# Optimization experiments

Hardware: AMD Instinct MI355X
Metric: run time of the kernel (lower is better)

Reference implementation:

```python
import jax, jax.numpy as jnp
import numpy as np

B, A, L, D, H = 8, 16, 80, 128, 6  # scenes, agents/scene, lanes/scene, feat dim, heads
LN_EPS = 1e-5


def _build_edges():
    hi_l, wi_l = [], []
    n_agt = B * A
    for b in range(B):
        ids = np.concatenate([np.arange(b * A, (b + 1) * A),
                              n_agt + np.arange(b * L, (b + 1) * L)])
        n = len(ids)
        hi_l.append(np.repeat(ids, n))  # 'd -> (d n)'
        wi_l.append(np.tile(ids, n))    # 'd -> (n d)'
    return (jnp.asarray(np.concatenate(hi_l), dtype=jnp.int32),
            jnp.asarray(np.concatenate(wi_l), dtype=jnp.int32))


def setup_inputs() -> dict:
    key = jax.random.key(0)
    ks = jax.random.split(key, 10)
    w = 0.05  # small init so exp(att) is well-behaved
    hi, wi = _build_edges()
    return {
        "agents": jax.random.normal(ks[0], (B * A, D), jnp.float32),
        "lanes": jax.random.normal(ks[1], (B * L, D), jnp.float32),
        "Wq": w * jax.random.normal(ks[2], (D, H * D), jnp.float32),
        "Wk": w * jax.random.normal(ks[3], (D, H * D), jnp.float32),
        "Wv": w * jax.random.normal(ks[4], (D, H * D), jnp.float32),
        "Wout1": w * jax.random.normal(ks[5], (H * D, D), jnp.float32),
        "Wout2": w * jax.random.normal(ks[6], (D, D), jnp.float32),
        "W1": w * jax.random.normal(ks[7], (D, D), jnp.float32),
        "ln_g": jnp.ones((D,), jnp.float32),
        "ln_b": jnp.zeros((D,), jnp.float32),
        "W2": w * jax.random.normal(ks[8], (D, D), jnp.float32),
        "hi": hi,
        "wi": wi,
    }


def _layernorm(x, g, b):
    mu = x.mean(-1, keepdims=True)
    var = ((x - mu) ** 2).mean(-1, keepdims=True)
    return (x - mu) * jax.lax.rsqrt(var + LN_EPS) * g + b


def reference(agents, lanes, Wq, Wk, Wv, Wout1, Wout2, W1, ln_g, ln_b, W2, hi, wi):
    nodes = jnp.concatenate([agents, lanes], axis=0)  # [N, D]
    N = nodes.shape[0]
    n_agt = agents.shape[0]
    scale = D ** -0.5

    src = nodes[hi]  # [E, D] (query side)
    dst = nodes[wi]  # [E, D] (key/value side)
    q = (src @ Wq).reshape(-1, H, D)
    k = (dst @ Wk).reshape(-1, H, D)
    v = jax.nn.relu(dst @ Wv).reshape(-1, H, D)

    att = jnp.einsum('ehd,ehd->eh', q, k) * scale          # [E, H]
    att = jnp.exp(att - att.max())                          # global-max-shifted exp (as in source)
    denom = jax.ops.segment_sum(att, hi, num_segments=N)    # [N, H]
    att = att / denom[hi]
    out = jax.ops.segment_sum(att[..., None] * v, hi, num_segments=N)  # [N, H, D]
    out = out.reshape(N, H * D)

    out = jax.nn.relu(out @ Wout1) @ Wout2                  # to_out
    h = _layernorm(nodes @ W1 + out, ln_g, ln_b)
    h = jax.nn.relu(h)
    h = h @ W2
    h = jax.nn.relu(h + nodes)                              # residual to pre-attention nodes
    return h[:n_agt]
```

## Files before the change

kernel.cpp:

```cpp
#include <hip/hip_runtime.h>
#include <math.h>

#define LN_EPS 1e-5f


__global__ __launch_bounds__(256) void k_qv(
    const float* __restrict__ agents, const float* __restrict__ lanes,
    const float* __restrict__ Wv, const float* __restrict__ Wq,
    const float* __restrict__ W1, float* __restrict__ V,
    float* __restrict__ Qb, float* __restrict__ base)
{
    __shared__ float As[128][68];
    __shared__ float Bs[128][68];

    const int tid = threadIdx.x;
    const int bid = blockIdx.x;

    const float* W;
    float* Out;
    int r0, wc0, wstride, dstride;
    bool dorelu = false;
    if (bid < 144) {
        const int br = bid % 12, bc = bid / 12;
        r0 = br * 64; W = Wv; wc0 = bc * 64; wstride = 768;
        Out = V; dstride = 768; dorelu = true;
    } else if (bid < 168) {
        const int idx = bid - 144;
        r0 = (idx & 1) * 64; W = Wq; wc0 = (idx >> 1) * 64; wstride = 768;
        Out = Qb; dstride = 768;
    } else {
        const int idx = bid - 168;
        r0 = (idx & 1) * 64; W = W1; wc0 = (idx >> 1) * 64; wstride = 128;
        Out = base; dstride = 128;
    }

    {
        const int row = tid >> 2, kv = tid & 3;
        const int gr = r0 + row;
        const float* src = (gr < 128) ? (agents + (size_t)gr * 128)
                                      : (lanes + (size_t)(gr - 128) * 128);
        #pragma unroll
        for (int j = 0; j < 8; ++j) {
            const int k0 = kv * 4 + j * 16;
            const float4 a = *(const float4*)(src + k0);
            As[k0 + 0][row] = a.x; As[k0 + 1][row] = a.y;
            As[k0 + 2][row] = a.z; As[k0 + 3][row] = a.w;
        }
    }
    {
        const int kr = tid >> 4, c4 = tid & 15;
        #pragma unroll
        for (int i = 0; i < 8; ++i) {
            const int k = kr + 16 * i;
            *(float4*)&Bs[k][c4 * 4] =
                *(const float4*)(W + (size_t)k * wstride + wc0 + c4 * 4);
        }
    }
    __syncthreads();

    const int tx = tid & 15, ty = tid >> 4;
    float acc[4][4] = {};
    #pragma unroll 8
    for (int k = 0; k < 128; ++k) {
        const float4 a = *(const float4*)&As[k][ty * 4];
        const float4 b = *(const float4*)&Bs[k][tx * 4];
        const float av[4] = {a.x, a.y, a.z, a.w};
        #pragma unroll
        for (int i = 0; i < 4; ++i) {
            acc[i][0] += av[i] * b.x; acc[i][1] += av[i] * b.y;
            acc[i][2] += av[i] * b.z; acc[i][3] += av[i] * b.w;
        }
    }
    #pragma unroll
    for (int i = 0; i < 4; ++i) {
        float4 v = make_float4(acc[i][0], acc[i][1], acc[i][2], acc[i][3]);
        if (dorelu) {
            v.x = fmaxf(v.x, 0.f); v.y = fmaxf(v.y, 0.f);
            v.z = fmaxf(v.z, 0.f); v.w = fmaxf(v.w, 0.f);
        }
        *(float4*)(Out + (size_t)(r0 + ty * 4 + i) * dstride + wc0 + tx * 4) = v;
    }
}

__global__ __launch_bounds__(512) void k_attn2(
    const float* __restrict__ agents, const float* __restrict__ lanes,
    const float* __restrict__ Wk, const float* __restrict__ V,
    const float* __restrict__ Qb, float* __restrict__ AO)
{
    __shared__ float Ns[96][132];
    __shared__ float Vh[96][68];
    __shared__ float Qs[16][132];
    __shared__ float Tt[16][132];
    __shared__ float Sm[16][100];
    __shared__ float Wc[32][132];

    const int tid = threadIdx.x;
    const int b = blockIdx.x;
    const int s = b / 12, r12 = b % 12;
    const int h = r12 >> 1, half = r12 & 1;

    #pragma unroll
    for (int ii = 0; ii < 6; ++ii) {
        const int idx = tid + ii * 512;
        const int n = idx >> 5, c4 = idx & 31;
        const float* src = (n < 16) ? (agents + (size_t)(s * 16 + n) * 128)
                                    : (lanes + (size_t)(s * 80 + n - 16) * 128);
        *(float4*)&Ns[n][c4 * 4] = *(const float4*)(src + c4 * 4);
    }
    #pragma unroll
    for (int ii = 0; ii < 3; ++ii) {
        const int idx = tid + ii * 512;
        const int n = idx >> 4, c4 = idx & 15;
        const int g = (n < 16) ? (s * 16 + n) : (128 + s * 80 + (n - 16));
        *(float4*)&Vh[n][c4 * 4] =
            *(const float4*)(V + (size_t)g * 768 + h * 128 + half * 64 + c4 * 4);
    }
    {
        const int r = tid >> 5, c4 = tid & 31;
        *(float4*)&Qs[r][c4 * 4] =
            *(const float4*)(Qb + (size_t)(s * 16 + r) * 768 + h * 128 + c4 * 4);
    }
    __syncthreads();

    const int r = tid >> 5, kc = tid & 31;
    for (int ck = 0; ck < 4; ++ck) {
        {
            const int i0 = tid * 2;
            #pragma unroll
            for (int ii = 0; ii < 2; ++ii) {
                const int idx = i0 + ii;
                const int row = idx >> 5, c4 = idx & 31;
                *(float4*)&Wc[row][c4 * 4] =
                    *(const float4*)(Wk + (size_t)(ck * 32 + row) * 768 +
                                     h * 128 + c4 * 4);
            }
        }
        __syncthreads();
        {
            float acc = 0.f;
            #pragma unroll 8
            for (int c4 = 0; c4 < 32; ++c4) {
                const float4 q = *(const float4*)&Qs[r][c4 * 4];
                const float4 w = *(const float4*)&Wc[kc][c4 * 4];
                acc += q.x * w.x + q.y * w.y + q.z * w.z + q.w * w.w;
            }
            Tt[r][ck * 32 + kc] = acc;
        }
        __syncthreads();
    }

    {
        const int i = r, jc = kc;
        float s0 = 0, s1 = 0, s2 = 0;
        #pragma unroll 4
        for (int kk = 0; kk < 32; ++kk) {
            const float4 t4 = *(const float4*)&Tt[i][kk * 4];
            const float4 a  = *(const float4*)&Ns[jc][kk * 4];
            const float4 bb = *(const float4*)&Ns[jc + 32][kk * 4];
            const float4 c  = *(const float4*)&Ns[jc + 64][kk * 4];
            s0 += t4.x*a.x  + t4.y*a.y  + t4.z*a.z  + t4.w*a.w;
            s1 += t4.x*bb.x + t4.y*bb.y + t4.z*bb.z + t4.w*bb.w;
            s2 += t4.x*c.x  + t4.y*c.y  + t4.z*c.z  + t4.w*c.w;
        }
        const float scale = 0.088388347648318447f;
        s0 *= scale; s1 *= scale; s2 *= scale;
        float m = fmaxf(fmaxf(s0, s1), s2);
        #pragma unroll
        for (int o = 16; o >= 1; o >>= 1) m = fmaxf(m, __shfl_xor(m, o, 32));
        const float e0 = __expf(s0 - m), e1 = __expf(s1 - m), e2 = __expf(s2 - m);
        float sum = e0 + e1 + e2;
        #pragma unroll
        for (int o = 16; o >= 1; o >>= 1) sum += __shfl_xor(sum, o, 32);
        const float inv = 1.0f / sum;
        Sm[i][jc]      = e0 * inv;
        Sm[i][jc + 32] = e1 * inv;
        Sm[i][jc + 64] = e2 * inv;
    }

    {
        const int i = r, d = kc;
        float o0 = 0, o1 = 0;
        #pragma unroll 4
        for (int j = 0; j < 96; ++j) {
            const float p = Sm[i][j];
            const float2 v = *(const float2*)&Vh[j][2 * d];
            o0 += p * v.x; o1 += p * v.y;
        }
        float* dst = AO + (size_t)(s * 16 + i) * 768 + h * 128 + half * 64 + 2 * d;
        *(float2*)dst = make_float2(o0, o1);
    }
}

__global__ __launch_bounds__(256) void k_f1w(
    const float* __restrict__ AO, const float* __restrict__ Wout1,
    float* __restrict__ y1p)
{
    __shared__ float As[64][68];
    __shared__ float Bs[64][68];

    const int tid = threadIdx.x;
    const int b = blockIdx.x;
    const int ks = b >> 2, quad = b & 3;
    const int m0 = (quad >> 1) * 64, n0 = (quad & 1) * 64;

    {
        const int row = tid >> 2, kq = tid & 3;
        #pragma unroll
        for (int j = 0; j < 4; ++j) {
            const int k0 = kq * 4 + j * 16;
            const float4 a =
                *(const float4*)(AO + (size_t)(m0 + row) * 768 + ks * 64 + k0);
            As[k0 + 0][row] = a.x; As[k0 + 1][row] = a.y;
            As[k0 + 2][row] = a.z; As[k0 + 3][row] = a.w;
        }
    }
    {
        const int kr = tid >> 4, c4 = tid & 15;
        #pragma unroll
        for (int i = 0; i < 4; ++i) {
            const int k = kr + 16 * i;
            *(float4*)&Bs[k][c4 * 4] =
                *(const float4*)(Wout1 + (size_t)(ks * 64 + k) * 128 + n0 + c4 * 4);
        }
    }
    __syncthreads();

    const int tx = tid & 15, ty = tid >> 4;
    float acc[4][4] = {};
    #pragma unroll 8
    for (int k = 0; k < 64; ++k) {
        const float4 a = *(const float4*)&As[k][ty * 4];
        const float4 bv = *(const float4*)&Bs[k][tx * 4];
        const float av[4] = {a.x, a.y, a.z, a.w};
        #pragma unroll
        for (int i = 0; i < 4; ++i) {
            acc[i][0] += av[i] * bv.x; acc[i][1] += av[i] * bv.y;
            acc[i][2] += av[i] * bv.z; acc[i][3] += av[i] * bv.w;
        }
    }
    float* dst = y1p + (size_t)ks * 16384 + (size_t)m0 * 128 + n0;
    #pragma unroll
    for (int i = 0; i < 4; ++i)
        *(float4*)(dst + (size_t)(ty * 4 + i) * 128 + tx * 4) =
            make_float4(acc[i][0], acc[i][1], acc[i][2], acc[i][3]);
}

__global__ __launch_bounds__(512) void k_f2(
    const float* __restrict__ y1p, const float* __restrict__ base,
    const float* __restrict__ agents, const float* __restrict__ Wout2,
    const float* __restrict__ ln_g, const float* __restrict__ ln_b,
    const float* __restrict__ W2, float* __restrict__ out)
{
    const int a = blockIdx.x;
    const int tid = threadIdx.x;
    __shared__ float y1s[128];
    __shared__ float nr[128];
    __shared__ float br[128];
    __shared__ float hb[128];
    __shared__ float ps[512];
    __shared__ float red[4];

    if (tid < 32) {
        float4 acc = make_float4(0,0,0,0);
        #pragma unroll
        for (int ks = 0; ks < 12; ++ks) {
            const float4 v =
                *(const float4*)(y1p + (size_t)ks * 16384 + (size_t)a * 128 + tid * 4);
            acc.x += v.x; acc.y += v.y; acc.z += v.z; acc.w += v.w;
        }
        y1s[tid * 4 + 0] = fmaxf(acc.x, 0.f); y1s[tid * 4 + 1] = fmaxf(acc.y, 0.f);
        y1s[tid * 4 + 2] = fmaxf(acc.z, 0.f); y1s[tid * 4 + 3] = fmaxf(acc.w, 0.f);
    } else if (tid < 64) {
        const int t = tid - 32;
        *(float4*)&nr[t * 4] = *(const float4*)(agents + (size_t)a * 128 + t * 4);
    } else if (tid < 96) {
        const int t = tid - 64;
        *(float4*)&br[t * 4] = *(const float4*)(base + (size_t)a * 128 + t * 4);
    }
    __syncthreads();

    const int d = tid & 127, g = tid >> 7;
    {
        const int k0 = g * 32;
        float p = 0.f;
        #pragma unroll 8
        for (int k = 0; k < 32; ++k)
            p += y1s[k0 + k] * Wout2[(size_t)(k0 + k) * 128 + d];
        ps[tid] = p;
    }
    __syncthreads();

    float tval = 0.f;
    if (tid < 128) tval = ps[d] + ps[128 + d] + ps[256 + d] + ps[384 + d] + br[d];
    float s1 = tval, s2 = tval * tval;
    #pragma unroll
    for (int o = 32; o >= 1; o >>= 1) { s1 += __shfl_xor(s1, o); s2 += __shfl_xor(s2, o); }
    if (tid < 128 && (tid & 63) == 0) {
        red[(tid >> 6) * 2] = s1; red[(tid >> 6) * 2 + 1] = s2;
    }
    __syncthreads();
    if (tid < 128) {
        const float S1 = red[0] + red[2], S2 = red[1] + red[3];
        const float mu  = S1 * (1.0f / 128.0f);
        const float var = S2 * (1.0f / 128.0f) - mu * mu;
        const float rin = rsqrtf(var + LN_EPS);
        hb[tid] = fmaxf((tval - mu) * rin * ln_g[tid] + ln_b[tid], 0.0f);
    }
    __syncthreads();

    {
        const int k0 = g * 32;
        float p = 0.f;
        #pragma unroll 8
        for (int k = 0; k < 32; ++k)
            p += hb[k0 + k] * W2[(size_t)(k0 + k) * 128 + d];
        ps[tid] = p;
    }
    __syncthreads();
    if (tid < 128)
        out[(size_t)a * 128 + d] =
            fmaxf(ps[d] + ps[128 + d] + ps[256 + d] + ps[384 + d] + nr[d], 0.0f);
}

extern "C" void kernel_launch(void* const* d_in, const int* in_sizes, int n_in,
                              void* d_out, int out_size, void* d_ws, size_t ws_size,
                              hipStream_t stream)
{
    const float* agents = (const float*)d_in[0];
    const float* lanes  = (const float*)d_in[1];
    const float* Wq     = (const float*)d_in[2];
    const float* Wk     = (const float*)d_in[3];
    const float* Wv     = (const float*)d_in[4];
    const float* Wout1  = (const float*)d_in[5];
    const float* Wout2  = (const float*)d_in[6];
    const float* W1     = (const float*)d_in[7];
    const float* ln_g   = (const float*)d_in[8];
    const float* ln_b   = (const float*)d_in[9];
    const float* W2     = (const float*)d_in[10];

    float* ws = (float*)d_ws;
    float* V    = ws;
    float* Qb   = V + 768 * 768;
    float* base = Qb + 128 * 768;
    float* AO   = base + 16384;
    float* y1p  = AO + 128 * 768;
    float* outp = (float*)d_out;

    k_qv   <<<172, 256, 0, stream>>>(agents, lanes, Wv, Wq, W1, V, Qb, base);
    k_attn2<<<96, 512, 0, stream>>>(agents, lanes, Wk, V, Qb, AO);
    k_f1w  <<<48, 256, 0, stream>>>(AO, Wout1, y1p);
    k_f2   <<<128, 512, 0, stream>>>(y1p, base, agents, Wout2, ln_g, ln_b, W2, outp);
}
```

Before: 108.6 us.

## Fuse all stages into one cooperative kernel with grid sync

Replaces the four launches with a single cooperative kernel. Each attention block now computes its own V and Q projections in shared memory instead of reading them from precomputed global buffers. A grid-wide sync follows, after which 64 blocks each run the Wout1/Wout2/W1/LayerNorm/W2 tail for two agents. This removes three launch boundaries and the V/Qb/base/y1p workspace traffic. In exchange, V is recomputed per head-half tile, the Wout1 GEMM runs on fewer blocks with uncoalesced-per-thread weight reads, and the grid sync adds cost.

```diff
diff --git a/kernel.cpp b/kernel.cpp
--- a/kernel.cpp
+++ b/kernel.cpp
@@ -1,325 +1,287 @@
 #include <hip/hip_runtime.h>
+#include <hip/hip_cooperative_groups.h>
 #include <math.h>
 
 #define LN_EPS 1e-5f
 
-
-__global__ __launch_bounds__(256) void k_qv(
+namespace cg = cooperative_groups;
+
+
+#define RELU4(v) do { (v).x=fmaxf((v).x,0.f); (v).y=fmaxf((v).y,0.f); \
+                      (v).z=fmaxf((v).z,0.f); (v).w=fmaxf((v).w,0.f); } while(0)
+
+__global__ __launch_bounds__(512) void k_fused(
     const float* __restrict__ agents, const float* __restrict__ lanes,
-    const float* __restrict__ Wv, const float* __restrict__ Wq,
-    const float* __restrict__ W1, float* __restrict__ V,
-    float* __restrict__ Qb, float* __restrict__ base)
+    const float* __restrict__ Wq, const float* __restrict__ Wk,
+    const float* __restrict__ Wv, const float* __restrict__ Wout1,
+    const float* __restrict__ Wout2, const float* __restrict__ W1,
+    const float* __restrict__ ln_g, const float* __restrict__ ln_b,
+    const float* __restrict__ W2, float* __restrict__ AO,
+    float* __restrict__ out)
 {
-    __shared__ float As[128][68];
-    __shared__ float Bs[128][68];
-
-    const int tid = threadIdx.x;
-    const int bid = blockIdx.x;
-
-    const float* W;
-    float* Out;
-    int r0, wc0, wstride, dstride;
-    bool dorelu = false;
-    if (bid < 144) {
-        const int br = bid % 12, bc = bid / 12;
-        r0 = br * 64; W = Wv; wc0 = bc * 64; wstride = 768;
-        Out = V; dstride = 768; dorelu = true;
-    } else if (bid < 168) {
-        const int idx = bid - 144;
-        r0 = (idx & 1) * 64; W = Wq; wc0 = (idx >> 1) * 64; wstride = 768;
-        Out = Qb; dstride = 768;
-    } else {
-        const int idx = bid - 168;
-        r0 = (idx & 1) * 64; W = W1; wc0 = (idx >> 1) * 64; wstride = 128;
-        Out = base; dstride = 128;
-    }
-
-    {
-        const int row = tid >> 2, kv = tid & 3;
-        const int gr = r0 + row;
-        const float* src = (gr < 128) ? (agents + (size_t)gr * 128)
-                                      : (lanes + (size_t)(gr - 128) * 128);
-        #pragma unroll
-        for (int j = 0; j < 8; ++j) {
-            const int k0 = kv * 4 + j * 16;
-            const float4 a = *(const float4*)(src + k0);
-            As[k0 + 0][row] = a.x; As[k0 + 1][row] = a.y;
-            As[k0 + 2][row] = a.z; As[k0 + 3][row] = a.w;
-        }
-    }
-    {
-        const int kr = tid >> 4, c4 = tid & 15;
-        #pragma unroll
-        for (int i = 0; i < 8; ++i) {
-            const int k = kr + 16 * i;
-            *(float4*)&Bs[k][c4 * 4] =
-                *(const float4*)(W + (size_t)k * wstride + wc0 + c4 * 4);
-        }
-    }
-    __syncthreads();
-
-    const int tx = tid & 15, ty = tid >> 4;
-    float acc[4][4] = {};
-    #pragma unroll 8
-    for (int k = 0; k < 128; ++k) {
-        const float4 a = *(const float4*)&As[k][ty * 4];
-        const float4 b = *(const float4*)&Bs[k][tx * 4];
-        const float av[4] = {a.x, a.y, a.z, a.w};
-        #pragma unroll
-        for (int i = 0; i < 4; ++i) {
-            acc[i][0] += av[i] * b.x; acc[i][1] += av[i] * b.y;
-            acc[i][2] += av[i] * b.z; acc[i][3] += av[i] * b.w;
-        }
-    }
-    #pragma unroll
-    for (int i = 0; i < 4; ++i) {
-        float4 v = make_float4(acc[i][0], acc[i][1], acc[i][2], acc[i][3]);
-        if (dorelu) {
-            v.x = fmaxf(v.x, 0.f); v.y = fmaxf(v.y, 0.f);
-            v.z = fmaxf(v.z, 0.f); v.w = fmaxf(v.w, 0.f);
-        }
-        *(float4*)(Out + (size_t)(r0 + ty * 4 + i) * dstride + wc0 + tx * 4) = v;
-    }
-}
-
-__global__ __launch_bounds__(512) void k_attn2(
-    const float* __restrict__ agents, const float* __restrict__ lanes,
-    const float* __restrict__ Wk, const float* __restrict__ V,
-    const float* __restrict__ Qb, float* __restrict__ AO)
-{
-    __shared__ float Ns[96][132];
-    __shared__ float Vh[96][68];
-    __shared__ float Qs[16][132];
-    __shared__ float Tt[16][132];
-    __shared__ float Sm[16][100];
-    __shared__ float Wc[32][132];
+    __shared__ float smem[29248];
 
     const int tid = threadIdx.x;
     const int b = blockIdx.x;
-    const int s = b / 12, r12 = b % 12;
-    const int h = r12 >> 1, half = r12 & 1;
-
-    #pragma unroll
-    for (int ii = 0; ii < 6; ++ii) {
-        const int idx = tid + ii * 512;
-        const int n = idx >> 5, c4 = idx & 31;
-        const float* src = (n < 16) ? (agents + (size_t)(s * 16 + n) * 128)
-                                    : (lanes + (size_t)(s * 80 + n - 16) * 128);
-        *(float4*)&Ns[n][c4 * 4] = *(const float4*)(src + c4 * 4);
-    }
-    #pragma unroll
-    for (int ii = 0; ii < 3; ++ii) {
-        const int idx = tid + ii * 512;
-        const int n = idx >> 4, c4 = idx & 15;
-        const int g = (n < 16) ? (s * 16 + n) : (128 + s * 80 + (n - 16));
-        *(float4*)&Vh[n][c4 * 4] =
-            *(const float4*)(V + (size_t)g * 768 + h * 128 + half * 64 + c4 * 4);
-    }
+
     {
-        const int r = tid >> 5, c4 = tid & 31;
-        *(float4*)&Qs[r][c4 * 4] =
-            *(const float4*)(Qb + (size_t)(s * 16 + r) * 768 + h * 128 + c4 * 4);
-    }
-    __syncthreads();
-
-    const int r = tid >> 5, kc = tid & 31;
-    for (int ck = 0; ck < 4; ++ck) {
-        {
-            const int i0 = tid * 2;
+        float (*Ns)[132] = (float (*)[132])(smem);
+        float (*Vh)[68]  = (float (*)[68]) (smem + 12672);
+        float (*Qs)[132] = (float (*)[132])(smem + 19200);
+        float (*Tt)[132] = (float (*)[132])(smem + 21312);
+        float (*Sm)[100] = (float (*)[100])(smem + 23424);
+        float (*Wc)[132] = (float (*)[132])(smem + 25024);
+
+        const int sc = b / 12, r12 = b % 12;
+        const int h = r12 >> 1, half = r12 & 1;
+
+        #pragma unroll
+        for (int ii = 0; ii < 6; ++ii) {
+            const int idx = tid + ii * 512;
+            const int n = idx >> 5, c4 = idx & 31;
+            const float* src = (n < 16) ? (agents + (size_t)(sc * 16 + n) * 128)
+                                        : (lanes + (size_t)(sc * 80 + n - 16) * 128);
+            *(float4*)&Ns[n][c4 * 4] = *(const float4*)(src + c4 * 4);
+        }
+
+        {
+            const int r = tid >> 4, c4 = tid & 15;
+            float4 acc0 = make_float4(0, 0, 0, 0);
+            float4 acc1 = make_float4(0, 0, 0, 0);
+            float4 acc2 = make_float4(0, 0, 0, 0);
+            for (int ck = 0; ck < 4; ++ck) {
+                *(float4*)&Wc[r][c4 * 4] = *(const float4*)(
+                    Wv + (size_t)(ck * 32 + r) * 768 + h * 128 + half * 64 + c4 * 4);
+                __syncthreads();
+                #pragma unroll
+                for (int kk = 0; kk < 8; ++kk) {
+                    const int k0 = ck * 32 + kk * 4;
+                    const float4 n0 = *(const float4*)&Ns[r     ][k0];
+                    const float4 n1 = *(const float4*)&Ns[r + 32][k0];
+                    const float4 n2 = *(const float4*)&Ns[r + 64][k0];
+                    const float a0[4] = {n0.x, n0.y, n0.z, n0.w};
+                    const float a1[4] = {n1.x, n1.y, n1.z, n1.w};
+                    const float a2[4] = {n2.x, n2.y, n2.z, n2.w};
+                    #pragma unroll
+                    for (int j = 0; j < 4; ++j) {
+                        const float4 w = *(const float4*)&Wc[kk * 4 + j][c4 * 4];
+                        acc0.x += a0[j]*w.x; acc0.y += a0[j]*w.y;
+                        acc0.z += a0[j]*w.z; acc0.w += a0[j]*w.w;
+                        acc1.x += a1[j]*w.x; acc1.y += a1[j]*w.y;
+                        acc1.z += a1[j]*w.z; acc1.w += a1[j]*w.w;
+                        acc2.x += a2[j]*w.x; acc2.y += a2[j]*w.y;
+                        acc2.z += a2[j]*w.z; acc2.w += a2[j]*w.w;
+                    }
+                }
+                __syncthreads();
+            }
+            RELU4(acc0); RELU4(acc1); RELU4(acc2);
+            *(float4*)&Vh[r     ][c4 * 4] = acc0;
+            *(float4*)&Vh[r + 32][c4 * 4] = acc1;
+            *(float4*)&Vh[r + 64][c4 * 4] = acc2;
+        }
+
+        {
+            const int r = tid >> 5, kc = tid & 31;
+            float4 acc = make_float4(0, 0, 0, 0);
+            for (int ck = 0; ck < 4; ++ck) {
+                #pragma unroll
+                for (int ii = 0; ii < 2; ++ii) {
+                    const int idx = tid * 2 + ii;
+                    const int row = idx >> 5, cc = idx & 31;
+                    *(float4*)&Wc[row][cc * 4] = *(const float4*)(
+                        Wq + (size_t)(ck * 32 + row) * 768 + h * 128 + cc * 4);
+                }
+                __syncthreads();
+                #pragma unroll
+                for (int kk = 0; kk < 8; ++kk) {
+                    const float4 qa = *(const float4*)&Ns[r][ck * 32 + kk * 4];
+                    const float av[4] = {qa.x, qa.y, qa.z, qa.w};
+                    #pragma unroll
+                    for (int j = 0; j < 4; ++j) {
+                        const float4 w = *(const float4*)&Wc[kk * 4 + j][kc * 4];
+                        acc.x += av[j]*w.x; acc.y += av[j]*w.y;
+                        acc.z += av[j]*w.z; acc.w += av[j]*w.w;
+                    }
+                }
+                __syncthreads();
+            }
+            *(float4*)&Qs[r][kc * 4] = acc;
+        }
+
+        const int r = tid >> 5, kc = tid & 31;
+        for (int ck = 0; ck < 4; ++ck) {
             #pragma unroll
             for (int ii = 0; ii < 2; ++ii) {
-                const int idx = i0 + ii;
-                const int row = idx >> 5, c4 = idx & 31;
-                *(float4*)&Wc[row][c4 * 4] =
-                    *(const float4*)(Wk + (size_t)(ck * 32 + row) * 768 +
-                                     h * 128 + c4 * 4);
-            }
-        }
-        __syncthreads();
-        {
-            float acc = 0.f;
+                const int idx = tid * 2 + ii;
+                const int row = idx >> 5, cc = idx & 31;
+                *(float4*)&Wc[row][cc * 4] = *(const float4*)(
+                    Wk + (size_t)(ck * 32 + row) * 768 + h * 128 + cc * 4);
+            }
+            __syncthreads();
+            {
+                float acc = 0.f;
+                #pragma unroll 8
+                for (int c4 = 0; c4 < 32; ++c4) {
+                    const float4 q = *(const float4*)&Qs[r][c4 * 4];
+                    const float4 w = *(const float4*)&Wc[kc][c4 * 4];
+                    acc += q.x*w.x + q.y*w.y + q.z*w.z + q.w*w.w;
+                }
+                Tt[r][ck * 32 + kc] = acc;
+            }
+            __syncthreads();
+        }
+
+        {
+            const int i = r, jc = kc;
+            float s0 = 0, s1 = 0, s2 = 0;
+            #pragma unroll 4
+            for (int kk = 0; kk < 32; ++kk) {
+                const float4 t4 = *(const float4*)&Tt[i][kk * 4];
+                const float4 a  = *(const float4*)&Ns[jc][kk * 4];
+                const float4 bb = *(const float4*)&Ns[jc + 32][kk * 4];
+                const float4 c  = *(const float4*)&Ns[jc + 64][kk * 4];
+                s0 += t4.x*a.x  + t4.y*a.y  + t4.z*a.z  + t4.w*a.w;
+                s1 += t4.x*bb.x + t4.y*bb.y + t4.z*bb.z + t4.w*bb.w;
+                s2 += t4.x*c.x  + t4.y*c.y  + t4.z*c.z  + t4.w*c.w;
+            }
+            const float scale = 0.088388347648318447f;
+            s0 *= scale; s1 *= scale; s2 *= scale;
+            float m = fmaxf(fmaxf(s0, s1), s2);
+            #pragma unroll
+            for (int o = 16; o >= 1; o >>= 1) m = fmaxf(m, __shfl_xor(m, o, 32));
+            const float e0 = __expf(s0 - m), e1 = __expf(s1 - m), e2 = __expf(s2 - m);
+            float sum = e0 + e1 + e2;
+            #pragma unroll
+            for (int o = 16; o >= 1; o >>= 1) sum += __shfl_xor(sum, o, 32);
+            const float inv = 1.0f / sum;
+            Sm[i][jc]      = e0 * inv;
+            Sm[i][jc + 32] = e1 * inv;
+            Sm[i][jc + 64] = e2 * inv;
+        }
+
+        {
+            const int i = r, dd = kc;
+            float o0 = 0, o1 = 0;
+            #pragma unroll 4
+            for (int j = 0; j < 96; ++j) {
+                const float p = Sm[i][j];
+                const float2 v = *(const float2*)&Vh[j][2 * dd];
+                o0 += p * v.x; o1 += p * v.y;
+            }
+            float* dst = AO + (size_t)(sc * 16 + i) * 768 + h * 128 + half * 64 + 2 * dd;
+            *(float2*)dst = make_float2(o0, o1);
+        }
+    }
+
+    __threadfence();
+    cg::this_grid().sync();
+
+    if (b < 64) {
+        float* ao0 = smem;
+        float* ao1 = smem + 768;
+        float* ps0 = smem + 1536;
+        float* ps1 = smem + 2048;
+        float* y10 = smem + 2560;
+        float* y11 = smem + 2688;
+        float* nr0 = smem + 2816;
+        float* nr1 = smem + 2944;
+        float* hb0 = smem + 3072;
+        float* hb1 = smem + 3200;
+        float* red = smem + 3328;
+
+        const int a0 = b * 2, a1 = b * 2 + 1;
+        if (tid < 192) {
+            *(float4*)&ao0[tid * 4] = *(const float4*)(AO + (size_t)a0 * 768 + tid * 4);
+        } else if (tid < 384) {
+            const int t = tid - 192;
+            *(float4*)&ao1[t * 4] = *(const float4*)(AO + (size_t)a1 * 768 + t * 4);
+        } else if (tid < 416) {
+            const int t = tid - 384;
+            *(float4*)&nr0[t * 4] = *(const float4*)(agents + (size_t)a0 * 128 + t * 4);
+        } else if (tid < 448) {
+            const int t = tid - 416;
+            *(float4*)&nr1[t * 4] = *(const float4*)(agents + (size_t)a1 * 128 + t * 4);
+        }
+        __syncthreads();
+
+        const int d = tid & 127, g = tid >> 7;
+        {
+            float p0 = 0.f, p1 = 0.f;
+            const int k0 = g * 192;
             #pragma unroll 8
-            for (int c4 = 0; c4 < 32; ++c4) {
-                const float4 q = *(const float4*)&Qs[r][c4 * 4];
-                const float4 w = *(const float4*)&Wc[kc][c4 * 4];
-                acc += q.x * w.x + q.y * w.y + q.z * w.z + q.w * w.w;
-            }
-            Tt[r][ck * 32 + kc] = acc;
-        }
-        __syncthreads();
+            for (int k = 0; k < 192; ++k) {
+                const float w = Wout1[(size_t)(k0 + k) * 128 + d];
+                p0 += ao0[k0 + k] * w; p1 += ao1[k0 + k] * w;
+            }
+            ps0[tid] = p0; ps1[tid] = p1;
+        }
+        __syncthreads();
+        if (tid < 128) {
+            y10[tid] = fmaxf(ps0[tid] + ps0[128 + tid] + ps0[256 + tid] + ps0[384 + tid], 0.f);
+            y11[tid] = fmaxf(ps1[tid] + ps1[128 + tid] + ps1[256 + tid] + ps1[384 + tid], 0.f);
+        }
+        __syncthreads();
+        {
+            float p0 = 0.f, p1 = 0.f;
+            const int k0 = g * 32;
+            #pragma unroll 8
+            for (int k = 0; k < 32; ++k) {
+                const float w2v = Wout2[(size_t)(k0 + k) * 128 + d];
+                const float w1v = W1[(size_t)(k0 + k) * 128 + d];
+                p0 += y10[k0 + k] * w2v + nr0[k0 + k] * w1v;
+                p1 += y11[k0 + k] * w2v + nr1[k0 + k] * w1v;
+            }
+            ps0[tid] = p0; ps1[tid] = p1;
+        }
+        __syncthreads();
+        float t0 = 0.f, t1 = 0.f;
+        if (tid < 128) {
+            t0 = ps0[d] + ps0[128 + d] + ps0[256 + d] + ps0[384 + d];
+            t1 = ps1[d] + ps1[128 + d] + ps1[256 + d] + ps1[384 + d];
+        }
+        float s10 = t0, s20 = t0 * t0, s11 = t1, s21 = t1 * t1;
+        #pragma unroll
+        for (int o = 32; o >= 1; o >>= 1) {
+            s10 += __shfl_xor(s10, o); s20 += __shfl_xor(s20, o);
+            s11 += __shfl_xor(s11, o); s21 += __shfl_xor(s21, o);
+        }
+        if (tid < 128 && (tid & 63) == 0) {
+            const int wid = tid >> 6;
+            red[wid * 4 + 0] = s10; red[wid * 4 + 1] = s20;
+            red[wid * 4 + 2] = s11; red[wid * 4 + 3] = s21;
+        }
+        __syncthreads();
+        if (tid < 128) {
+            const float S10 = red[0] + red[4], S20 = red[1] + red[5];
+            const float S11 = red[2] + red[6], S21 = red[3] + red[7];
+            const float mu0 = S10 * (1.0f / 128.0f);
+            const float var0 = S20 * (1.0f / 128.0f) - mu0 * mu0;
+            const float mu1 = S11 * (1.0f / 128.0f);
+            const float var1 = S21 * (1.0f / 128.0f) - mu1 * mu1;
+            const float g_ = ln_g[tid], b_ = ln_b[tid];
+            hb0[tid] = fmaxf((t0 - mu0) * rsqrtf(var0 + LN_EPS) * g_ + b_, 0.0f);
+            hb1[tid] = fmaxf((t1 - mu1) * rsqrtf(var1 + LN_EPS) * g_ + b_, 0.0f);
+        }
+        __syncthreads();
+        {
+            float p0 = 0.f, p1 = 0.f;
+            const int k0 = g * 32;
+            #pragma unroll 8
+            for (int k = 0; k < 32; ++k) {
+                const float w = W2[(size_t)(k0 + k) * 128 + d];
+                p0 += hb0[k0 + k] * w; p1 += hb1[k0 + k] * w;
+            }
+            ps0[tid] = p0; ps1[tid] = p1;
+        }
+        __syncthreads();
+        if (tid < 128) {
+            out[(size_t)a0 * 128 + d] =
+                fmaxf(ps0[d] + ps0[128 + d] + ps0[256 + d] + ps0[384 + d] + nr0[d], 0.0f);
+            out[(size_t)a1 * 128 + d] =
+                fmaxf(ps1[d] + ps1[128 + d] + ps1[256 + d] + ps1[384 + d] + nr1[d], 0.0f);
+        }
     }
-
-    {
-        const int i = r, jc = kc;
-        float s0 = 0, s1 = 0, s2 = 0;
-        #pragma unroll 4
-        for (int kk = 0; kk < 32; ++kk) {
-            const float4 t4 = *(const float4*)&Tt[i][kk * 4];
-            const float4 a  = *(const float4*)&Ns[jc][kk * 4];
-            const float4 bb = *(const float4*)&Ns[jc + 32][kk * 4];
-            const float4 c  = *(const float4*)&Ns[jc + 64][kk * 4];
-            s0 += t4.x*a.x  + t4.y*a.y  + t4.z*a.z  + t4.w*a.w;
-            s1 += t4.x*bb.x + t4.y*bb.y + t4.z*bb.z + t4.w*bb.w;
-            s2 += t4.x*c.x  + t4.y*c.y  + t4.z*c.z  + t4.w*c.w;
-        }
-        const float scale = 0.088388347648318447f;
-        s0 *= scale; s1 *= scale; s2 *= scale;
-        float m = fmaxf(fmaxf(s0, s1), s2);
-        #pragma unroll
-        for (int o = 16; o >= 1; o >>= 1) m = fmaxf(m, __shfl_xor(m, o, 32));
-        const float e0 = __expf(s0 - m), e1 = __expf(s1 - m), e2 = __expf(s2 - m);
-        float sum = e0 + e1 + e2;
-        #pragma unroll
-        for (int o = 16; o >= 1; o >>= 1) sum += __shfl_xor(sum, o, 32);
-        const float inv = 1.0f / sum;
-        Sm[i][jc]      = e0 * inv;
-        Sm[i][jc + 32] = e1 * inv;
-        Sm[i][jc + 64] = e2 * inv;
-    }
-
-    {
-        const int i = r, d = kc;
-        float o0 = 0, o1 = 0;
-        #pragma unroll 4
-        for (int j = 0; j < 96; ++j) {
-            const float p = Sm[i][j];
-            const float2 v = *(const float2*)&Vh[j][2 * d];
-            o0 += p * v.x; o1 += p * v.y;
-        }
-        float* dst = AO + (size_t)(s * 16 + i) * 768 + h * 128 + half * 64 + 2 * d;
-        *(float2*)dst = make_float2(o0, o1);
-    }
-}
-
-__global__ __launch_bounds__(256) void k_f1w(
-    const float* __restrict__ AO, const float* __restrict__ Wout1,
-    float* __restrict__ y1p)
-{
-    __shared__ float As[64][68];
-    __shared__ float Bs[64][68];
-
-    const int tid = threadIdx.x;
-    const int b = blockIdx.x;
-    const int ks = b >> 2, quad = b & 3;
-    const int m0 = (quad >> 1) * 64, n0 = (quad & 1) * 64;
-
-    {
-        const int row = tid >> 2, kq = tid & 3;
-        #pragma unroll
-        for (int j = 0; j < 4; ++j) {
-            const int k0 = kq * 4 + j * 16;
-            const float4 a =
-                *(const float4*)(AO + (size_t)(m0 + row) * 768 + ks * 64 + k0);
-            As[k0 + 0][row] = a.x; As[k0 + 1][row] = a.y;
-            As[k0 + 2][row] = a.z; As[k0 + 3][row] = a.w;
-        }
-    }
-    {
-        const int kr = tid >> 4, c4 = tid & 15;
-        #pragma unroll
-        for (int i = 0; i < 4; ++i) {
-            const int k = kr + 16 * i;
-            *(float4*)&Bs[k][c4 * 4] =
-                *(const float4*)(Wout1 + (size_t)(ks * 64 + k) * 128 + n0 + c4 * 4);
-        }
-    }
-    __syncthreads();
-
-    const int tx = tid & 15, ty = tid >> 4;
-    float acc[4][4] = {};
-    #pragma unroll 8
-    for (int k = 0; k < 64; ++k) {
-        const float4 a = *(const float4*)&As[k][ty * 4];
-        const float4 bv = *(const float4*)&Bs[k][tx * 4];
-        const float av[4] = {a.x, a.y, a.z, a.w};
-        #pragma unroll
-        for (int i = 0; i < 4; ++i) {
-            acc[i][0] += av[i] * bv.x; acc[i][1] += av[i] * bv.y;
-            acc[i][2] += av[i] * bv.z; acc[i][3] += av[i] * bv.w;
-        }
-    }
-    float* dst = y1p + (size_t)ks * 16384 + (size_t)m0 * 128 + n0;
-    #pragma unroll
-    for (int i = 0; i < 4; ++i)
-        *(float4*)(dst + (size_t)(ty * 4 + i) * 128 + tx * 4) =
-            make_float4(acc[i][0], acc[i][1], acc[i][2], acc[i][3]);
-}
-
-__global__ __launch_bounds__(512) void k_f2(
-    const float* __restrict__ y1p, const float* __restrict__ base,
-    const float* __restrict__ agents, const float* __restrict__ Wout2,
-    const float* __restrict__ ln_g, const float* __restrict__ ln_b,
-    const float* __restrict__ W2, float* __restrict__ out)
-{
-    const int a = blockIdx.x;
-    const int tid = threadIdx.x;
-    __shared__ float y1s[128];
-    __shared__ float nr[128];
-    __shared__ float br[128];
-    __shared__ float hb[128];
-    __shared__ float ps[512];
-    __shared__ float red[4];
-
-    if (tid < 32) {
-        float4 acc = make_float4(0,0,0,0);
-        #pragma unroll
-        for (int ks = 0; ks < 12; ++ks) {
-            const float4 v =
-                *(const float4*)(y1p + (size_t)ks * 16384 + (size_t)a * 128 + tid * 4);
-            acc.x += v.x; acc.y += v.y; acc.z += v.z; acc.w += v.w;
-        }
-        y1s[tid * 4 + 0] = fmaxf(acc.x, 0.f); y1s[tid * 4 + 1] = fmaxf(acc.y, 0.f);
-        y1s[tid * 4 + 2] = fmaxf(acc.z, 0.f); y1s[tid * 4 + 3] = fmaxf(acc.w, 0.f);
-    } else if (tid < 64) {
-        const int t = tid - 32;
-        *(float4*)&nr[t * 4] = *(const float4*)(agents + (size_t)a * 128 + t * 4);
-    } else if (tid < 96) {
-        const int t = tid - 64;
-        *(float4*)&br[t * 4] = *(const float4*)(base + (size_t)a * 128 + t * 4);
-    }
-    __syncthreads();
-
-    const int d = tid & 127, g = tid >> 7;
-    {
-        const int k0 = g * 32;
-        float p = 0.f;
-        #pragma unroll 8
-        for (int k = 0; k < 32; ++k)
-            p += y1s[k0 + k] * Wout2[(size_t)(k0 + k) * 128 + d];
-        ps[tid] = p;
-    }
-    __syncthreads();
-
-    float tval = 0.f;
-    if (tid < 128) tval = ps[d] + ps[128 + d] + ps[256 + d] + ps[384 + d] + br[d];
-    float s1 = tval, s2 = tval * tval;
-    #pragma unroll
-    for (int o = 32; o >= 1; o >>= 1) { s1 += __shfl_xor(s1, o); s2 += __shfl_xor(s2, o); }
-    if (tid < 128 && (tid & 63) == 0) {
-        red[(tid >> 6) * 2] = s1; red[(tid >> 6) * 2 + 1] = s2;
-    }
-    __syncthreads();
-    if (tid < 128) {
-        const float S1 = red[0] + red[2], S2 = red[1] + red[3];
-        const float mu  = S1 * (1.0f / 128.0f);
-        const float var = S2 * (1.0f / 128.0f) - mu * mu;
-        const float rin = rsqrtf(var + LN_EPS);
-        hb[tid] = fmaxf((tval - mu) * rin * ln_g[tid] + ln_b[tid], 0.0f);
-    }
-    __syncthreads();
-
-    {
-        const int k0 = g * 32;
-        float p = 0.f;
-        #pragma unroll 8
-        for (int k = 0; k < 32; ++k)
-            p += hb[k0 + k] * W2[(size_t)(k0 + k) * 128 + d];
-        ps[tid] = p;
-    }
-    __syncthreads();
-    if (tid < 128)
-        out[(size_t)a * 128 + d] =
-            fmaxf(ps[d] + ps[128 + d] + ps[256 + d] + ps[384 + d] + nr[d], 0.0f);
 }
 
 extern "C" void kernel_launch(void* const* d_in, const int* in_sizes, int n_in,
@@ -338,16 +300,11 @@
     const float* ln_b   = (const float*)d_in[9];
     const float* W2     = (const float*)d_in[10];
 
-    float* ws = (float*)d_ws;
-    float* V    = ws;
-    float* Qb   = V + 768 * 768;
-    float* base = Qb + 128 * 768;
-    float* AO   = base + 16384;
-    float* y1p  = AO + 128 * 768;
+    float* AO   = (float*)d_ws;
     float* outp = (float*)d_out;
 
-    k_qv   <<<172, 256, 0, stream>>>(agents, lanes, Wv, Wq, W1, V, Qb, base);
-    k_attn2<<<96, 512, 0, stream>>>(agents, lanes, Wk, V, Qb, AO);
-    k_f1w  <<<48, 256, 0, stream>>>(AO, Wout1, y1p);
-    k_f2   <<<128, 512, 0, stream>>>(y1p, base, agents, Wout2, ln_g, ln_b, W2, outp);
+    void* args[] = {&agents, &lanes, &Wq, &Wk, &Wv, &Wout1, &Wout2, &W1,
+                    &ln_g, &ln_b, &W2, &AO, &outp};
+    hipLaunchCooperativeKernel((void*)k_fused, dim3(96), dim3(512),
+                               args, 0, stream);
 }
```

After: 174.4 us. +60.5%, slower.

## Fuse Wout1 projection and tail into one kernel; restructure attention Wk staging

Applied to the files above, without the earlier changes.

Merges the split-K Wout1 GEMM and the LayerNorm/W2 tail into one per-agent kernel, which also computes nodes@W1 inline instead of in the QV kernel. This drops one launch and the partial-sum workspace round trip. The attention kernel now loads the whole Wk head slice at once instead of in four synchronized chunks, and uses register-tiled 4x4 micro-kernels on fewer threads. The cost is that each tail block streams all of Wout1 itself, and more of the attention work runs on a subset of its threads.

```diff
diff --git a/kernel.cpp b/kernel.cpp
--- a/kernel.cpp
+++ b/kernel.cpp
@@ -7,8 +7,7 @@
 __global__ __launch_bounds__(256) void k_qv(
     const float* __restrict__ agents, const float* __restrict__ lanes,
     const float* __restrict__ Wv, const float* __restrict__ Wq,
-    const float* __restrict__ W1, float* __restrict__ V,
-    float* __restrict__ Qb, float* __restrict__ base)
+    float* __restrict__ V, float* __restrict__ Qb)
 {
     __shared__ float As[128][68];
     __shared__ float Bs[128][68];
@@ -18,20 +17,16 @@
 
     const float* W;
     float* Out;
-    int r0, wc0, wstride, dstride;
+    int r0, wc0;
     bool dorelu = false;
     if (bid < 144) {
         const int br = bid % 12, bc = bid / 12;
-        r0 = br * 64; W = Wv; wc0 = bc * 64; wstride = 768;
-        Out = V; dstride = 768; dorelu = true;
-    } else if (bid < 168) {
+        r0 = br * 64; W = Wv; wc0 = bc * 64;
+        Out = V; dorelu = true;
+    } else {
         const int idx = bid - 144;
-        r0 = (idx & 1) * 64; W = Wq; wc0 = (idx >> 1) * 64; wstride = 768;
-        Out = Qb; dstride = 768;
-    } else {
-        const int idx = bid - 168;
-        r0 = (idx & 1) * 64; W = W1; wc0 = (idx >> 1) * 64; wstride = 128;
-        Out = base; dstride = 128;
+        r0 = (idx & 1) * 64; W = Wq; wc0 = (idx >> 1) * 64;
+        Out = Qb;
     }
 
     {
@@ -53,7 +48,7 @@
         for (int i = 0; i < 8; ++i) {
             const int k = kr + 16 * i;
             *(float4*)&Bs[k][c4 * 4] =
-                *(const float4*)(W + (size_t)k * wstride + wc0 + c4 * 4);
+                *(const float4*)(W + (size_t)k * 768 + wc0 + c4 * 4);
         }
     }
     __syncthreads();
@@ -78,21 +73,21 @@
             v.x = fmaxf(v.x, 0.f); v.y = fmaxf(v.y, 0.f);
             v.z = fmaxf(v.z, 0.f); v.w = fmaxf(v.w, 0.f);
         }
-        *(float4*)(Out + (size_t)(r0 + ty * 4 + i) * dstride + wc0 + tx * 4) = v;
+        *(float4*)(Out + (size_t)(r0 + ty * 4 + i) * 768 + wc0 + tx * 4) = v;
     }
 }
 
-__global__ __launch_bounds__(512) void k_attn2(
+__global__ __launch_bounds__(512) void k_attn(
     const float* __restrict__ agents, const float* __restrict__ lanes,
     const float* __restrict__ Wk, const float* __restrict__ V,
     const float* __restrict__ Qb, float* __restrict__ AO)
 {
     __shared__ float Ns[96][132];
-    __shared__ float Vh[96][68];
+    __shared__ float Vh[96][64];
     __shared__ float Qs[16][132];
     __shared__ float Tt[16][132];
-    __shared__ float Sm[16][100];
-    __shared__ float Wc[32][132];
+    __shared__ float Wks[128][132];
+    float (*Sm)[100] = (float (*)[100])&Wks[0][0];
 
     const int tid = threadIdx.x;
     const int b = blockIdx.x;
@@ -108,6 +103,13 @@
         *(float4*)&Ns[n][c4 * 4] = *(const float4*)(src + c4 * 4);
     }
     #pragma unroll
+    for (int ii = 0; ii < 8; ++ii) {
+        const int idx = tid + ii * 512;
+        const int row = idx >> 5, c4 = idx & 31;
+        *(float4*)&Wks[row][c4 * 4] =
+            *(const float4*)(Wk + (size_t)row * 768 + h * 128 + c4 * 4);
+    }
+    #pragma unroll
     for (int ii = 0; ii < 3; ++ii) {
         const int idx = tid + ii * 512;
         const int n = idx >> 4, c4 = idx & 15;
@@ -122,176 +124,154 @@
     }
     __syncthreads();
 
-    const int r = tid >> 5, kc = tid & 31;
-    for (int ck = 0; ck < 4; ++ck) {
-        {
-            const int i0 = tid * 2;
-            #pragma unroll
-            for (int ii = 0; ii < 2; ++ii) {
-                const int idx = i0 + ii;
-                const int row = idx >> 5, c4 = idx & 31;
-                *(float4*)&Wc[row][c4 * 4] =
-                    *(const float4*)(Wk + (size_t)(ck * 32 + row) * 768 +
-                                     h * 128 + c4 * 4);
-            }
-        }
-        __syncthreads();
-        {
-            float acc = 0.f;
-            #pragma unroll 8
-            for (int c4 = 0; c4 < 32; ++c4) {
-                const float4 q = *(const float4*)&Qs[r][c4 * 4];
-                const float4 w = *(const float4*)&Wc[kc][c4 * 4];
-                acc += q.x * w.x + q.y * w.y + q.z * w.z + q.w * w.w;
-            }
-            Tt[r][ck * 32 + kc] = acc;
-        }
-        __syncthreads();
-    }
-
-    {
-        const int i = r, jc = kc;
-        float s0 = 0, s1 = 0, s2 = 0;
+    if (tid < 128) {
+        const int kc = tid & 31, rq = tid >> 5;
+        float acc[4][4] = {};
+        #pragma unroll 4
+        for (int c4 = 0; c4 < 32; ++c4) {
+            float4 q[4], w[4];
+            #pragma unroll
+            for (int u = 0; u < 4; ++u)
+                q[u] = *(const float4*)&Qs[rq + 4 * u][c4 * 4];
+            #pragma unroll
+            for (int u = 0; u < 4; ++u)
+                w[u] = *(const float4*)&Wks[kc + 32 * u][c4 * 4];
+            #pragma unroll
+            for (int ur = 0; ur < 4; ++ur)
+                #pragma unroll
+                for (int uk = 0; uk < 4; ++uk)
+                    acc[ur][uk] += q[ur].x * w[uk].x + q[ur].y * w[uk].y
+                                 + q[ur].z * w[uk].z + q[ur].w * w[uk].w;
+        }
+        #pragma unroll
+        for (int ur = 0; ur < 4; ++ur)
+            #pragma unroll
+            for (int uk = 0; uk < 4; ++uk)
+                Tt[rq + 4 * ur][kc + 32 * uk] = acc[ur][uk];
+    }
+    __syncthreads();
+
+    if (tid < 128) {
+        const int jc = tid & 31, iq = tid >> 5;
+        float s0[4] = {}, s1[4] = {}, s2[4] = {};
         #pragma unroll 4
         for (int kk = 0; kk < 32; ++kk) {
-            const float4 t4 = *(const float4*)&Tt[i][kk * 4];
-            const float4 a  = *(const float4*)&Ns[jc][kk * 4];
-            const float4 bb = *(const float4*)&Ns[jc + 32][kk * 4];
-            const float4 c  = *(const float4*)&Ns[jc + 64][kk * 4];
-            s0 += t4.x*a.x  + t4.y*a.y  + t4.z*a.z  + t4.w*a.w;
-            s1 += t4.x*bb.x + t4.y*bb.y + t4.z*bb.z + t4.w*bb.w;
-            s2 += t4.x*c.x  + t4.y*c.y  + t4.z*c.z  + t4.w*c.w;
+            float4 t[4];
+            #pragma unroll
+            for (int u = 0; u < 4; ++u)
+                t[u] = *(const float4*)&Tt[iq + 4 * u][kk * 4];
+            const float4 n0 = *(const float4*)&Ns[jc][kk * 4];
+            const float4 n1 = *(const float4*)&Ns[jc + 32][kk * 4];
+            const float4 n2 = *(const float4*)&Ns[jc + 64][kk * 4];
+            #pragma unroll
+            for (int u = 0; u < 4; ++u) {
+                s0[u] += t[u].x*n0.x + t[u].y*n0.y + t[u].z*n0.z + t[u].w*n0.w;
+                s1[u] += t[u].x*n1.x + t[u].y*n1.y + t[u].z*n1.z + t[u].w*n1.w;
+                s2[u] += t[u].x*n2.x + t[u].y*n2.y + t[u].z*n2.z + t[u].w*n2.w;
+            }
         }
         const float scale = 0.088388347648318447f;
-        s0 *= scale; s1 *= scale; s2 *= scale;
-        float m = fmaxf(fmaxf(s0, s1), s2);
-        #pragma unroll
-        for (int o = 16; o >= 1; o >>= 1) m = fmaxf(m, __shfl_xor(m, o, 32));
-        const float e0 = __expf(s0 - m), e1 = __expf(s1 - m), e2 = __expf(s2 - m);
-        float sum = e0 + e1 + e2;
-        #pragma unroll
-        for (int o = 16; o >= 1; o >>= 1) sum += __shfl_xor(sum, o, 32);
-        const float inv = 1.0f / sum;
-        Sm[i][jc]      = e0 * inv;
-        Sm[i][jc + 32] = e1 * inv;
-        Sm[i][jc + 64] = e2 * inv;
-    }
-
-    {
-        const int i = r, d = kc;
-        float o0 = 0, o1 = 0;
-        #pragma unroll 4
+        #pragma unroll
+        for (int u = 0; u < 4; ++u) {
+            const float a0 = s0[u] * scale, a1 = s1[u] * scale, a2 = s2[u] * scale;
+            float m = fmaxf(fmaxf(a0, a1), a2);
+            #pragma unroll
+            for (int o = 16; o >= 1; o >>= 1) m = fmaxf(m, __shfl_xor(m, o, 32));
+            const float e0 = __expf(a0 - m), e1 = __expf(a1 - m), e2 = __expf(a2 - m);
+            float sum = e0 + e1 + e2;
+            #pragma unroll
+            for (int o = 16; o >= 1; o >>= 1) sum += __shfl_xor(sum, o, 32);
+            const float inv = 1.0f / sum;
+            Sm[iq + 4 * u][jc]      = e0 * inv;
+            Sm[iq + 4 * u][jc + 32] = e1 * inv;
+            Sm[iq + 4 * u][jc + 64] = e2 * inv;
+        }
+    }
+    __syncthreads();
+
+    if (tid < 64) {
+        const int d4 = tid & 15, iq = tid >> 4;
+        float4 acc[4] = {};
+        #pragma unroll 2
         for (int j = 0; j < 96; ++j) {
-            const float p = Sm[i][j];
-            const float2 v = *(const float2*)&Vh[j][2 * d];
-            o0 += p * v.x; o1 += p * v.y;
-        }
-        float* dst = AO + (size_t)(s * 16 + i) * 768 + h * 128 + half * 64 + 2 * d;
-        *(float2*)dst = make_float2(o0, o1);
+            const float4 v = *(const float4*)&Vh[j][d4 * 4];
+            #pragma unroll
+            for (int u = 0; u < 4; ++u) {
+                const float p = Sm[iq + 4 * u][j];
+                acc[u].x += p * v.x; acc[u].y += p * v.y;
+                acc[u].z += p * v.z; acc[u].w += p * v.w;
+            }
+        }
+        #pragma unroll
+        for (int u = 0; u < 4; ++u)
+            *(float4*)(AO + (size_t)(s * 16 + iq + 4 * u) * 768 +
+                       h * 128 + half * 64 + d4 * 4) = acc[u];
     }
 }
 
-__global__ __launch_bounds__(256) void k_f1w(
-    const float* __restrict__ AO, const float* __restrict__ Wout1,
-    float* __restrict__ y1p)
+__global__ __launch_bounds__(512) void k_tail(
+    const float* __restrict__ AO, const float* __restrict__ agents,
+    const float* __restrict__ Wout1, const float* __restrict__ Wout2,
+    const float* __restrict__ W1, const float* __restrict__ ln_g,
+    const float* __restrict__ ln_b, const float* __restrict__ W2,
+    float* __restrict__ out)
 {
-    __shared__ float As[64][68];
-    __shared__ float Bs[64][68];
-
-    const int tid = threadIdx.x;
-    const int b = blockIdx.x;
-    const int ks = b >> 2, quad = b & 3;
-    const int m0 = (quad >> 1) * 64, n0 = (quad & 1) * 64;
-
-    {
-        const int row = tid >> 2, kq = tid & 3;
-        #pragma unroll
-        for (int j = 0; j < 4; ++j) {
-            const int k0 = kq * 4 + j * 16;
-            const float4 a =
-                *(const float4*)(AO + (size_t)(m0 + row) * 768 + ks * 64 + k0);
-            As[k0 + 0][row] = a.x; As[k0 + 1][row] = a.y;
-            As[k0 + 2][row] = a.z; As[k0 + 3][row] = a.w;
-        }
-    }
-    {
-        const int kr = tid >> 4, c4 = tid & 15;
-        #pragma unroll
-        for (int i = 0; i < 4; ++i) {
-            const int k = kr + 16 * i;
-            *(float4*)&Bs[k][c4 * 4] =
-                *(const float4*)(Wout1 + (size_t)(ks * 64 + k) * 128 + n0 + c4 * 4);
-        }
-    }
-    __syncthreads();
-
-    const int tx = tid & 15, ty = tid >> 4;
-    float acc[4][4] = {};
-    #pragma unroll 8
-    for (int k = 0; k < 64; ++k) {
-        const float4 a = *(const float4*)&As[k][ty * 4];
-        const float4 bv = *(const float4*)&Bs[k][tx * 4];
-        const float av[4] = {a.x, a.y, a.z, a.w};
-        #pragma unroll
-        for (int i = 0; i < 4; ++i) {
-            acc[i][0] += av[i] * bv.x; acc[i][1] += av[i] * bv.y;
-            acc[i][2] += av[i] * bv.z; acc[i][3] += av[i] * bv.w;
-        }
-    }
-    float* dst = y1p + (size_t)ks * 16384 + (size_t)m0 * 128 + n0;
-    #pragma unroll
-    for (int i = 0; i < 4; ++i)
-        *(float4*)(dst + (size_t)(ty * 4 + i) * 128 + tx * 4) =
-            make_float4(acc[i][0], acc[i][1], acc[i][2], acc[i][3]);
-}
-
-__global__ __launch_bounds__(512) void k_f2(
-    const float* __restrict__ y1p, const float* __restrict__ base,
-    const float* __restrict__ agents, const float* __restrict__ Wout2,
-    const float* __restrict__ ln_g, const float* __restrict__ ln_b,
-    const float* __restrict__ W2, float* __restrict__ out)
-{
-    const int a = blockIdx.x;
-    const int tid = threadIdx.x;
+    __shared__ float ao[768];
+    __shared__ float nrs[128];
+    __shared__ float ps[2048];
     __shared__ float y1s[128];
-    __shared__ float nr[128];
-    __shared__ float br[128];
     __shared__ float hb[128];
-    __shared__ float ps[512];
     __shared__ float red[4];
 
-    if (tid < 32) {
-        float4 acc = make_float4(0,0,0,0);
-        #pragma unroll
-        for (int ks = 0; ks < 12; ++ks) {
-            const float4 v =
-                *(const float4*)(y1p + (size_t)ks * 16384 + (size_t)a * 128 + tid * 4);
-            acc.x += v.x; acc.y += v.y; acc.z += v.z; acc.w += v.w;
-        }
-        y1s[tid * 4 + 0] = fmaxf(acc.x, 0.f); y1s[tid * 4 + 1] = fmaxf(acc.y, 0.f);
-        y1s[tid * 4 + 2] = fmaxf(acc.z, 0.f); y1s[tid * 4 + 3] = fmaxf(acc.w, 0.f);
-    } else if (tid < 64) {
-        const int t = tid - 32;
-        *(float4*)&nr[t * 4] = *(const float4*)(agents + (size_t)a * 128 + t * 4);
-    } else if (tid < 96) {
-        const int t = tid - 64;
-        *(float4*)&br[t * 4] = *(const float4*)(base + (size_t)a * 128 + t * 4);
-    }
-    __syncthreads();
-
-    const int d = tid & 127, g = tid >> 7;
-    {
-        const int k0 = g * 32;
-        float p = 0.f;
+    const int a = blockIdx.x, tid = threadIdx.x;
+    if (tid < 192) {
+        *(float4*)&ao[tid * 4] = *(const float4*)(AO + (size_t)a * 768 + tid * 4);
+    } else if (tid < 224) {
+        const int t = tid - 192;
+        *(float4*)&nrs[t * 4] = *(const float4*)(agents + (size_t)a * 128 + t * 4);
+    }
+    __syncthreads();
+
+    const int d4 = tid & 31, g = tid >> 5;
+    {
+        float4 acc = make_float4(0, 0, 0, 0);
+        const int k0 = g * 48;
         #pragma unroll 8
-        for (int k = 0; k < 32; ++k)
-            p += y1s[k0 + k] * Wout2[(size_t)(k0 + k) * 128 + d];
-        ps[tid] = p;
-    }
-    __syncthreads();
-
+        for (int k = 0; k < 48; ++k) {
+            const float av = ao[k0 + k];
+            const float4 w = *(const float4*)(Wout1 + (size_t)(k0 + k) * 128 + d4 * 4);
+            acc.x += av * w.x; acc.y += av * w.y;
+            acc.z += av * w.z; acc.w += av * w.w;
+        }
+        *(float4*)&ps[g * 128 + d4 * 4] = acc;
+    }
+    __syncthreads();
+    if (tid < 128) {
+        float ssum = 0.f;
+        #pragma unroll
+        for (int gg = 0; gg < 16; ++gg) ssum += ps[gg * 128 + tid];
+        y1s[tid] = fmaxf(ssum, 0.f);
+    }
+    __syncthreads();
+    {
+        float4 acc = make_float4(0, 0, 0, 0);
+        const int k0 = g * 8;
+        #pragma unroll
+        for (int k = 0; k < 8; ++k) {
+            const float yv = y1s[k0 + k], nv = nrs[k0 + k];
+            const float4 w2v = *(const float4*)(Wout2 + (size_t)(k0 + k) * 128 + d4 * 4);
+            const float4 w1v = *(const float4*)(W1 + (size_t)(k0 + k) * 128 + d4 * 4);
+            acc.x += yv * w2v.x + nv * w1v.x; acc.y += yv * w2v.y + nv * w1v.y;
+            acc.z += yv * w2v.z + nv * w1v.z; acc.w += yv * w2v.w + nv * w1v.w;
+        }
+        *(float4*)&ps[g * 128 + d4 * 4] = acc;
+    }
+    __syncthreads();
     float tval = 0.f;
-    if (tid < 128) tval = ps[d] + ps[128 + d] + ps[256 + d] + ps[384 + d] + br[d];
+    if (tid < 128) {
+        #pragma unroll
+        for (int gg = 0; gg < 16; ++gg) tval += ps[gg * 128 + tid];
+    }
     float s1 = tval, s2 = tval * tval;
     #pragma unroll
     for (int o = 32; o >= 1; o >>= 1) { s1 += __shfl_xor(s1, o); s2 += __shfl_xor(s2, o); }
@@ -303,23 +283,28 @@
         const float S1 = red[0] + red[2], S2 = red[1] + red[3];
         const float mu  = S1 * (1.0f / 128.0f);
         const float var = S2 * (1.0f / 128.0f) - mu * mu;
-        const float rin = rsqrtf(var + LN_EPS);
-        hb[tid] = fmaxf((tval - mu) * rin * ln_g[tid] + ln_b[tid], 0.0f);
-    }
-    __syncthreads();
-
-    {
-        const int k0 = g * 32;
-        float p = 0.f;
-        #pragma unroll 8
-        for (int k = 0; k < 32; ++k)
-            p += hb[k0 + k] * W2[(size_t)(k0 + k) * 128 + d];
-        ps[tid] = p;
-    }
-    __syncthreads();
-    if (tid < 128)
-        out[(size_t)a * 128 + d] =
-            fmaxf(ps[d] + ps[128 + d] + ps[256 + d] + ps[384 + d] + nr[d], 0.0f);
+        hb[tid] = fmaxf((tval - mu) * rsqrtf(var + LN_EPS) * ln_g[tid] + ln_b[tid], 0.f);
+    }
+    __syncthreads();
+    {
+        float4 acc = make_float4(0, 0, 0, 0);
+        const int k0 = g * 8;
+        #pragma unroll
+        for (int k = 0; k < 8; ++k) {
+            const float hv = hb[k0 + k];
+            const float4 w = *(const float4*)(W2 + (size_t)(k0 + k) * 128 + d4 * 4);
+            acc.x += hv * w.x; acc.y += hv * w.y;
+            acc.z += hv * w.z; acc.w += hv * w.w;
+        }
+        *(float4*)&ps[g * 128 + d4 * 4] = acc;
+    }
+    __syncthreads();
+    if (tid < 128) {
+        float o_ = nrs[tid];
+        #pragma unroll
+        for (int gg = 0; gg < 16; ++gg) o_ += ps[gg * 128 + tid];
+        out[(size_t)a * 128 + tid] = fmaxf(o_, 0.f);
+    }
 }
 
 extern "C" void kernel_launch(void* const* d_in, const int* in_sizes, int n_in,
@@ -341,13 +326,10 @@
     float* ws = (float*)d_ws;
     float* V    = ws;
     float* Qb   = V + 768 * 768;
-    float* base = Qb + 128 * 768;
-    float* AO   = base + 16384;
-    float* y1p  = AO + 128 * 768;
+    float* AO   = Qb + 128 * 768;
     float* outp = (float*)d_out;
 
-    k_qv   <<<172, 256, 0, stream>>>(agents, lanes, Wv, Wq, W1, V, Qb, base);
-    k_attn2<<<96, 512, 0, stream>>>(agents, lanes, Wk, V, Qb, AO);
-    k_f1w  <<<48, 256, 0, stream>>>(AO, Wout1, y1p);
-    k_f2   <<<128, 512, 0, stream>>>(y1p, base, agents, Wout2, ln_g, ln_b, W2, outp);
+    k_qv  <<<168, 256, 0, stream>>>(agents, lanes, Wv, Wq, V, Qb);
+    k_attn<<<96, 512, 0, stream>>>(agents, lanes, Wk, V, Qb, AO);
+    k_tail<<<128, 512, 0, stream>>>(AO, agents, Wout1, Wout2, W1, ln_g, ln_b, W2, outp);
 }
```

New measurement: 112.4 us. +3.5%, slower.
